# Performance work log

Measured on AMD Instinct MI355X. Metric: run time of the kernel, lower is better.

Reference implementation:

```python
import jax, jax.numpy as jnp
import numpy as np
import math

NUM_HEADS = 12
LN_EPS = 1e-5


def _band_mask(seq_len, level):
    # level 0 -> +/-2 window, level 1 -> +/-5 window, else full attention
    if level == 0:
        w = 2
    elif level == 1:
        w = 5
    else:
        return jnp.zeros((seq_len, seq_len), dtype=jnp.float32)
    i = jnp.arange(seq_len)
    inside = jnp.abs(i[:, None] - i[None, :]) <= w
    return jnp.where(inside, 0.0, -jnp.inf).astype(jnp.float32)


def setup_inputs() -> dict:
    key = jax.random.key(0)
    ks = jax.random.split(key, 8)
    B, S, H = 8, 1000, 768
    init = 0.02
    return {
        "features": jax.random.normal(ks[0], (B, S, H), jnp.float32),
        "pos_emb": jax.random.normal(ks[1], (1000, H), jnp.float32) * init,
        "Wq": jax.random.normal(ks[2], (H, H), jnp.float32) * init,
        "bq": jnp.zeros((H,), jnp.float32),
        "Wk": jax.random.normal(ks[3], (H, H), jnp.float32) * init,
        "bk": jnp.zeros((H,), jnp.float32),
        "Wv": jax.random.normal(ks[4], (H, H), jnp.float32) * init,
        "bv": jnp.zeros((H,), jnp.float32),
        "Wo": jax.random.normal(ks[5], (H, H), jnp.float32) * init,
        "bo": jnp.zeros((H,), jnp.float32),
        "ln_g": jnp.ones((H,), jnp.float32),
        "ln_b": jnp.zeros((H,), jnp.float32),
        "level": 0,
    }


def reference(features, pos_emb, Wq, bq, Wk, bk, Wv, bv, Wo, bo, ln_g, ln_b, level):
    B, S, H = features.shape
    nh = NUM_HEADS
    hd = H // nh
    # level-specific positional encoding (level_specific=True path)
    scale = 1.0 + 0.1 * level
    x = features + pos_emb[:S][None, :, :] * scale

    def proj(W, b):
        y = jnp.einsum('bsh,oh->bso', x, W) + b  # torch Linear: x @ W.T + b
        return y.reshape(B, S, nh, hd).transpose(0, 2, 1, 3)  # [B, nh, S, hd]

    Q = proj(Wq, bq)
    K = proj(Wk, bk)
    V = proj(Wv, bv)

    scores = jnp.einsum('bhqd,bhkd->bhqk', Q, K) / math.sqrt(hd)
    scores = scores + _band_mask(S, level)[None, None, :, :]
    attn = jax.nn.softmax(scores, axis=-1)  # dropout is identity (eval / p=0)
    ctx = jnp.einsum('bhqk,bhkd->bhqd', attn, V)
    ctx = ctx.transpose(0, 2, 1, 3).reshape(B, S, H)

    out = jnp.einsum('bsh,oh->bso', ctx, Wo) + bo
    y = out + features
    mu = jnp.mean(y, axis=-1, keepdims=True)
    var = jnp.var(y, axis=-1, keepdims=True)
    return (y - mu) / jnp.sqrt(var + LN_EPS) * ln_g + ln_b
```

## Files before the change

### kernel.cpp

```cpp
#include <hip/hip_runtime.h>
#include <hip/hip_bf16.h>
#include <cstddef>

typedef __attribute__((ext_vector_type(8))) short bf16x8;
typedef __attribute__((ext_vector_type(4))) float f32x4;

static __device__ __forceinline__ unsigned short f2bf(float f) {
    unsigned int u = __float_as_uint(f);
    u += 0x7fffu + ((u >> 16) & 1u);
    return (unsigned short)(u >> 16);
}
static __device__ __forceinline__ float bf2f(unsigned short h) {
    return __uint_as_float(((unsigned int)h) << 16);
}

#define B_ 8
#define S_ 1000
#define H_ 768
#define NH_ 12
#define HD_ 64
#define M_ 8000
#define HC_ 2304

__global__ __launch_bounds__(256)
void prep_all_kernel(const float* __restrict__ feat, const float* __restrict__ pos,
                     const int* __restrict__ level, unsigned short* __restrict__ xb,
                     const float* __restrict__ wq, const float* __restrict__ wk,
                     const float* __restrict__ wv, const float* __restrict__ wo,
                     unsigned short* __restrict__ wdst) {
    const size_t NX = (size_t)M_ * H_ / 4;
    const size_t WSZ = (size_t)H_ * H_;
    size_t gid = (size_t)blockIdx.x * blockDim.x + threadIdx.x;
    if (gid < NX) {
        size_t e = gid * 4;
        float sc = 1.0f + 0.1f * (float)level[0];
        const float4 f = *reinterpret_cast<const float4*>(&feat[e]);
        size_t pe = e % ((size_t)S_ * H_);
        const float4 p = *reinterpret_cast<const float4*>(&pos[pe]);
        ushort4 o;
        o.x = f2bf(f.x + sc * p.x);
        o.y = f2bf(f.y + sc * p.y);
        o.z = f2bf(f.z + sc * p.z);
        o.w = f2bf(f.w + sc * p.w);
        *reinterpret_cast<ushort4*>(&xb[e]) = o;
    } else {
        size_t e = (gid - NX) * 4;
        if (e >= 4 * WSZ) return;
        const float* src; size_t off;
        if (e < WSZ)          { src = wq; off = e; }
        else if (e < 2 * WSZ) { src = wk; off = e - WSZ; }
        else if (e < 3 * WSZ) { src = wv; off = e - 2 * WSZ; }
        else                  { src = wo; off = e - 3 * WSZ; }
        const float4 f = *reinterpret_cast<const float4*>(&src[off]);
        ushort4 o;
        o.x = f2bf(f.x); o.y = f2bf(f.y); o.z = f2bf(f.z); o.w = f2bf(f.w);
        *reinterpret_cast<ushort4*>(&wdst[e]) = o;
    }
}

__global__ __launch_bounds__(512, 4)
void gemm_qkv5(const unsigned short* __restrict__ A,
               const unsigned short* __restrict__ Bw,
               const float* __restrict__ b0, const float* __restrict__ b1,
               const float* __restrict__ b2,
               unsigned short* __restrict__ outB) {
    const int K = H_;
    __shared__ char lds[65536];
    const int tid = threadIdx.x, lane = tid & 63, wid = tid >> 6;
    const int wr = wid >> 2, wc = wid & 3;
    const int fr = lane & 15, fq = lane >> 4;

    const int nwg = gridDim.x;
    const int q = nwg >> 3, r = nwg & 7;
    const int xcd = blockIdx.x & 7, idx = blockIdx.x >> 3;
    const int swz = (xcd < r) ? (xcd * (q + 1) + idx) : (r * (q + 1) + (xcd - r) * q + idx);
    const int ntn = HC_ / 128;
    const int bm = (swz / ntn) * 128;
    const int bn = (swz % ntn) * 128;

    const int srow = lane >> 2;
    const int scol = ((lane & 3) ^ ((lane >> 3) & 3)) * 8;

    auto stage = [&](int buf, int k0) {
        char* base = lds + buf * 32768;
#pragma unroll
        for (int s = 0; s < 2; ++s) {
            char* half = base + s * 16384;
            const int kk = k0 + s * 32;
            int ar = bm + wid * 16 + srow;
            ar = ar < M_ ? ar : M_ - 1;
            __builtin_amdgcn_global_load_lds(
                (const __attribute__((address_space(1))) unsigned int*)(A + (size_t)ar * K + kk + scol),
                (__attribute__((address_space(3))) unsigned int*)(half + wid * 1024), 16, 0, 0);
            const int br = bn + wid * 16 + srow;
            __builtin_amdgcn_global_load_lds(
                (const __attribute__((address_space(1))) unsigned int*)(Bw + (size_t)br * K + kk + scol),
                (__attribute__((address_space(3))) unsigned int*)(half + 8192 + wid * 1024), 16, 0, 0);
        }
    };

    f32x4 acc[4][2] = {};
    const int rsl = fq ^ ((fr >> 1) & 3);
    const int NT = K / 64;

    stage(0, 0);
    for (int t = 0; t < NT; ++t) {
        const int cur = t & 1;
        if (t + 1 < NT) {
            stage(cur ^ 1, (t + 1) * 64);
            asm volatile("s_waitcnt vmcnt(4)" ::: "memory");
        } else {
            asm volatile("s_waitcnt vmcnt(0)" ::: "memory");
        }
        __builtin_amdgcn_s_barrier();

        char* base = lds + cur * 32768;
#pragma unroll
        for (int s = 0; s < 2; ++s) {
            char* half = base + s * 16384;
            bf16x8 af[4], bfv[2];
#pragma unroll
            for (int m = 0; m < 4; ++m) {
                const int row = wr * 64 + m * 16 + fr;
                af[m] = *reinterpret_cast<const bf16x8*>(half + row * 64 + rsl * 16);
            }
#pragma unroll
            for (int n = 0; n < 2; ++n) {
                const int row = wc * 32 + n * 16 + fr;
                bfv[n] = *reinterpret_cast<const bf16x8*>(half + 8192 + row * 64 + rsl * 16);
            }
            __builtin_amdgcn_s_setprio(1);
#pragma unroll
            for (int m = 0; m < 4; ++m)
#pragma unroll
                for (int n = 0; n < 2; ++n)
                    acc[m][n] = __builtin_amdgcn_mfma_f32_16x16x32_bf16(bfv[n], af[m], acc[m][n], 0, 0, 0);
            __builtin_amdgcn_s_setprio(0);
        }
        __builtin_amdgcn_s_barrier();
    }

    const int colg = (bn < 768) ? bn : (bn < 1536) ? bn - 768 : bn - 1536;
    const float* bsel = (bn < 768) ? b0 : (bn < 1536) ? b1 : b2;
#pragma unroll
    for (int m = 0; m < 4; ++m) {
        const int row = bm + wr * 64 + m * 16 + fr;
        if (row >= M_) continue;
#pragma unroll
        for (int n = 0; n < 2; ++n) {
            const int cb = wc * 32 + n * 16 + fq * 4;
            const float4 bv = *reinterpret_cast<const float4*>(&bsel[colg + cb]);
            ushort4 o;
            o.x = f2bf(acc[m][n][0] + bv.x);
            o.y = f2bf(acc[m][n][1] + bv.y);
            o.z = f2bf(acc[m][n][2] + bv.z);
            o.w = f2bf(acc[m][n][3] + bv.w);
            *reinterpret_cast<ushort4*>(&outB[(size_t)row * HC_ + bn + cb]) = o;
        }
    }
}

__global__ __launch_bounds__(256, 4)
void gemm_out4(const unsigned short* __restrict__ A,
               const unsigned short* __restrict__ Bw,
               const float* __restrict__ b0,
               const float* __restrict__ resid,
               float* __restrict__ outF) {
    const int K = H_;
    __shared__ char lds[49152];
    const int tid = threadIdx.x, lane = tid & 63, wid = tid >> 6;
    const int wr = wid >> 1, wc = wid & 1;
    const int fr = lane & 15, fq = lane >> 4;

    const int nwg = gridDim.x;
    const int q = nwg >> 3, r = nwg & 7;
    const int xcd = blockIdx.x & 7, idx = blockIdx.x >> 3;
    const int swz = (xcd < r) ? (xcd * (q + 1) + idx) : (r * (q + 1) + (xcd - r) * q + idx);
    const int ntn = H_ / 64;
    const int bm = (swz / ntn) * 128;
    const int bn = (swz % ntn) * 64;

    const int srow = lane >> 2;
    const int scol = ((lane & 3) ^ ((lane >> 3) & 3)) * 8;

    auto stage = [&](int buf, int k0) {
        char* base = lds + buf * 24576;
#pragma unroll
        for (int s = 0; s < 2; ++s) {
            char* half = base + s * 12288;
            const int kk = k0 + s * 32;
#pragma unroll
            for (int t = 0; t < 2; ++t) {
                const int c = wid * 2 + t;
                int ar = bm + c * 16 + srow;
                ar = ar < M_ ? ar : M_ - 1;
                __builtin_amdgcn_global_load_lds(
                    (const __attribute__((address_space(1))) unsigned int*)(A + (size_t)ar * K + kk + scol),
                    (__attribute__((address_space(3))) unsigned int*)(half + c * 1024), 16, 0, 0);
            }
            const int br = bn + wid * 16 + srow;
            __builtin_amdgcn_global_load_lds(
                (const __attribute__((address_space(1))) unsigned int*)(Bw + (size_t)br * K + kk + scol),
                (__attribute__((address_space(3))) unsigned int*)(half + 8192 + wid * 1024), 16, 0, 0);
        }
    };

    f32x4 acc[4][2] = {};
    const int rsl = fq ^ ((fr >> 1) & 3);
    const int NT = K / 64;

    stage(0, 0);
    for (int t = 0; t < NT; ++t) {
        const int cur = t & 1;
        if (t + 1 < NT) {
            stage(cur ^ 1, (t + 1) * 64);
            asm volatile("s_waitcnt vmcnt(6)" ::: "memory");
        } else {
            asm volatile("s_waitcnt vmcnt(0)" ::: "memory");
        }
        __builtin_amdgcn_s_barrier();

        char* base = lds + cur * 24576;
#pragma unroll
        for (int s = 0; s < 2; ++s) {
            char* half = base + s * 12288;
            bf16x8 af[4], bfv[2];
#pragma unroll
            for (int m = 0; m < 4; ++m) {
                const int row = wr * 64 + m * 16 + fr;
                af[m] = *reinterpret_cast<const bf16x8*>(half + row * 64 + rsl * 16);
            }
#pragma unroll
            for (int n = 0; n < 2; ++n) {
                const int row = wc * 32 + n * 16 + fr;
                bfv[n] = *reinterpret_cast<const bf16x8*>(half + 8192 + row * 64 + rsl * 16);
            }
            __builtin_amdgcn_s_setprio(1);
#pragma unroll
            for (int m = 0; m < 4; ++m)
#pragma unroll
                for (int n = 0; n < 2; ++n)
                    acc[m][n] = __builtin_amdgcn_mfma_f32_16x16x32_bf16(bfv[n], af[m], acc[m][n], 0, 0, 0);
            __builtin_amdgcn_s_setprio(0);
        }
        __builtin_amdgcn_s_barrier();
    }

#pragma unroll
    for (int m = 0; m < 4; ++m) {
        const int row = bm + wr * 64 + m * 16 + fr;
        if (row >= M_) continue;
#pragma unroll
        for (int n = 0; n < 2; ++n) {
            const int col = bn + wc * 32 + n * 16 + fq * 4;
            const float4 bv = *reinterpret_cast<const float4*>(&b0[col]);
            const float4 rv = *reinterpret_cast<const float4*>(&resid[(size_t)row * H_ + col]);
            float4 ov;
            ov.x = acc[m][n][0] + bv.x + rv.x;
            ov.y = acc[m][n][1] + bv.y + rv.y;
            ov.z = acc[m][n][2] + bv.z + rv.z;
            ov.w = acc[m][n][3] + bv.w + rv.w;
            *reinterpret_cast<float4*>(&outF[(size_t)row * H_ + col]) = ov;
        }
    }
}

__global__ __launch_bounds__(256)
void attn_kernel(const unsigned short* __restrict__ QKV,
                 unsigned short* __restrict__ ctx,
                 const int* __restrict__ level_p) {
    const int lane = threadIdx.x & 63;
    const int wv = threadIdx.x >> 6;
    const int qiw = lane >> 2;
    const int d0 = (lane & 3) * 16;

    const int qt = blockIdx.x & 15;
    const int h  = (blockIdx.x >> 4) % NH_;
    const int b  = blockIdx.x / (16 * NH_);
    const int i  = qt * 64 + wv * 16 + qiw;
    const bool valid = i < S_;
    const int iq = valid ? i : S_ - 1;

    const int lev = level_p[0];
    const int w = (lev == 0) ? 2 : (lev == 1) ? 5 : S_;

    const size_t qoff = (size_t)(b * S_ + iq) * HC_ + h * HD_ + d0;
    bf16x8 qa = *reinterpret_cast<const bf16x8*>(&QKV[qoff]);
    bf16x8 qb = *reinterpret_cast<const bf16x8*>(&QKV[qoff + 8]);
    float qf[16];
#pragma unroll
    for (int t = 0; t < 8; ++t) {
        qf[t]     = bf2f((unsigned short)qa[t]);
        qf[t + 8] = bf2f((unsigned short)qb[t]);
    }

    const int j0 = max(0, i - w), j1 = min(S_ - 1, i + w);
    float mx = -1e30f, l = 0.f;
    float acc[16];
#pragma unroll
    for (int t = 0; t < 16; ++t) acc[t] = 0.f;

    for (int jc = j0; jc <= j1; jc += 5) {
        float s[5];
        int jj[5];
#pragma unroll
        for (int t = 0; t < 5; ++t) {
            const int j = jc + t;
            jj[t] = j <= j1 ? j : j1;
            const size_t koff = (size_t)(b * S_ + jj[t]) * HC_ + 768 + h * HD_ + d0;
            bf16x8 ka = *reinterpret_cast<const bf16x8*>(&QKV[koff]);
            bf16x8 kb = *reinterpret_cast<const bf16x8*>(&QKV[koff + 8]);
            float p = 0.f;
#pragma unroll
            for (int d = 0; d < 8; ++d) {
                p = fmaf(qf[d], bf2f((unsigned short)ka[d]), p);
                p = fmaf(qf[d + 8], bf2f((unsigned short)kb[d]), p);
            }
            s[t] = p;
        }
#pragma unroll
        for (int t = 0; t < 5; ++t) s[t] += __shfl_xor(s[t], 1);
#pragma unroll
        for (int t = 0; t < 5; ++t) s[t] += __shfl_xor(s[t], 2);
#pragma unroll
        for (int t = 0; t < 5; ++t)
            s[t] = (jc + t <= j1) ? s[t] * 0.125f : -1e30f;

        float cm = fmaxf(fmaxf(fmaxf(s[0], s[1]), fmaxf(s[2], s[3])), s[4]);
        float nm = fmaxf(mx, cm);
        float corr = __expf(mx - nm);
        l *= corr;
#pragma unroll
        for (int t = 0; t < 16; ++t) acc[t] *= corr;
#pragma unroll
        for (int t = 0; t < 5; ++t) {
            const float e = __expf(s[t] - nm);
            l += e;
            const size_t voff = (size_t)(b * S_ + jj[t]) * HC_ + 1536 + h * HD_ + d0;
            bf16x8 va = *reinterpret_cast<const bf16x8*>(&QKV[voff]);
            bf16x8 vb = *reinterpret_cast<const bf16x8*>(&QKV[voff + 8]);
#pragma unroll
            for (int d = 0; d < 8; ++d) {
                acc[d]     = fmaf(e, bf2f((unsigned short)va[d]), acc[d]);
                acc[d + 8] = fmaf(e, bf2f((unsigned short)vb[d]), acc[d + 8]);
            }
        }
        mx = nm;
    }

    if (valid) {
        const float inv = 1.f / l;
        bf16x8 o0, o1;
#pragma unroll
        for (int t = 0; t < 8; ++t) {
            o0[t] = (short)f2bf(acc[t] * inv);
            o1[t] = (short)f2bf(acc[t + 8] * inv);
        }
        unsigned short* dst = &ctx[(size_t)(b * S_ + i) * H_ + h * HD_ + d0];
        *reinterpret_cast<bf16x8*>(dst) = o0;
        *reinterpret_cast<bf16x8*>(dst + 8) = o1;
    }
}

__global__ __launch_bounds__(256)
void ln_kernel(float* __restrict__ y, const float* __restrict__ g, const float* __restrict__ bta) {
    int row = blockIdx.x;
    int tid = threadIdx.x;
    float* p = y + (size_t)row * H_;
    float v[3];
    float s = 0.f, s2 = 0.f;
#pragma unroll
    for (int t = 0; t < 3; ++t) {
        v[t] = p[tid + t * 256];
        s += v[t];
        s2 += v[t] * v[t];
    }
#pragma unroll
    for (int o = 32; o; o >>= 1) {
        s  += __shfl_xor(s, o);
        s2 += __shfl_xor(s2, o);
    }
    __shared__ float ss[4], ss2[4];
    if ((tid & 63) == 0) { ss[tid >> 6] = s; ss2[tid >> 6] = s2; }
    __syncthreads();
    s  = ss[0] + ss[1] + ss[2] + ss[3];
    s2 = ss2[0] + ss2[1] + ss2[2] + ss2[3];
    float mu = s * (1.f / H_);
    float var = s2 * (1.f / H_) - mu * mu;
    float rs = rsqrtf(var + 1e-5f);
#pragma unroll
    for (int t = 0; t < 3; ++t) {
        int c = tid + t * 256;
        p[c] = (v[t] - mu) * rs * g[c] + bta[c];
    }
}

extern "C" void kernel_launch(void* const* d_in, const int* in_sizes, int n_in,
                              void* d_out, int out_size, void* d_ws, size_t ws_size,
                              hipStream_t stream) {
    const float* feat  = (const float*)d_in[0];
    const float* pos   = (const float*)d_in[1];
    const float* Wq    = (const float*)d_in[2];
    const float* bq    = (const float*)d_in[3];
    const float* Wk    = (const float*)d_in[4];
    const float* bk    = (const float*)d_in[5];
    const float* Wv    = (const float*)d_in[6];
    const float* bv    = (const float*)d_in[7];
    const float* Wo    = (const float*)d_in[8];
    const float* bo    = (const float*)d_in[9];
    const float* ln_g  = (const float*)d_in[10];
    const float* ln_b  = (const float*)d_in[11];
    const int*   level = (const int*)d_in[12];
    float* out = (float*)d_out;

    char* ws = (char*)d_ws;
    unsigned short* xb   = (unsigned short*)ws;
    unsigned short* Wcat = xb + (size_t)M_ * H_;
    unsigned short* QKVb = Wcat + (size_t)4 * H_ * H_;
    unsigned short* ctxb = QKVb + (size_t)M_ * HC_;

    const int nprep = (int)(((size_t)M_ * H_ / 4 + (size_t)4 * H_ * H_ / 4 + 255) / 256);
    prep_all_kernel<<<nprep, 256, 0, stream>>>(feat, pos, level, xb, Wq, Wk, Wv, Wo, Wcat);
    gemm_qkv5<<<63 * 18, 512, 0, stream>>>(xb, Wcat, bq, bk, bv, QKVb);
    attn_kernel<<<B_ * NH_ * 16, 256, 0, stream>>>(QKVb, ctxb, level);
    gemm_out4<<<63 * 12, 256, 0, stream>>>(ctxb, Wcat + (size_t)3 * H_ * H_, bo, feat, out);
    ln_kernel<<<M_, 256, 0, stream>>>(out, ln_g, ln_b);
}
```

Baseline: 106.8 us.

## Use a four-slot LDS ring with three-deep prefetch in QKV GEMM

Replaces the double-buffered 64-wide K loop in the QKV projection GEMM with a four-slot ring of 32-wide K stages. Loads for stage p+3 are issued right after the fragment reads for stage p. Each step then needs one barrier instead of two. The aim is to hide global-to-LDS latency behind more in-flight loads and to cut barrier stalls, at the cost of more loop iterations and finer-grained waitcnt bookkeeping.

New measurement: 108.4 us. No clear change (+1.5%).

```diff
diff --git a/kernel.cpp b/kernel.cpp
--- a/kernel.cpp
+++ b/kernel.cpp
@@ -59,7 +59,7 @@
 }
 
 __global__ __launch_bounds__(512, 4)
-void gemm_qkv5(const unsigned short* __restrict__ A,
+void gemm_qkv7(const unsigned short* __restrict__ A,
                const unsigned short* __restrict__ Bw,
                const float* __restrict__ b0, const float* __restrict__ b1,
                const float* __restrict__ b2,
@@ -81,63 +81,53 @@
     const int srow = lane >> 2;
     const int scol = ((lane & 3) ^ ((lane >> 3) & 3)) * 8;
 
-    auto stage = [&](int buf, int k0) {
-        char* base = lds + buf * 32768;
-#pragma unroll
-        for (int s = 0; s < 2; ++s) {
-            char* half = base + s * 16384;
-            const int kk = k0 + s * 32;
-            int ar = bm + wid * 16 + srow;
-            ar = ar < M_ ? ar : M_ - 1;
-            __builtin_amdgcn_global_load_lds(
-                (const __attribute__((address_space(1))) unsigned int*)(A + (size_t)ar * K + kk + scol),
-                (__attribute__((address_space(3))) unsigned int*)(half + wid * 1024), 16, 0, 0);
-            const int br = bn + wid * 16 + srow;
-            __builtin_amdgcn_global_load_lds(
-                (const __attribute__((address_space(1))) unsigned int*)(Bw + (size_t)br * K + kk + scol),
-                (__attribute__((address_space(3))) unsigned int*)(half + 8192 + wid * 1024), 16, 0, 0);
-        }
+    auto stage = [&](int p) {
+        char* base = lds + (p & 3) * 16384;
+        const int kk = p * 32;
+        int ar = bm + wid * 16 + srow;
+        ar = ar < M_ ? ar : M_ - 1;
+        __builtin_amdgcn_global_load_lds(
+            (const __attribute__((address_space(1))) unsigned int*)(A + (size_t)ar * K + kk + scol),
+            (__attribute__((address_space(3))) unsigned int*)(base + wid * 1024), 16, 0, 0);
+        const int br = bn + wid * 16 + srow;
+        __builtin_amdgcn_global_load_lds(
+            (const __attribute__((address_space(1))) unsigned int*)(Bw + (size_t)br * K + kk + scol),
+            (__attribute__((address_space(3))) unsigned int*)(base + 8192 + wid * 1024), 16, 0, 0);
     };
 
     f32x4 acc[4][2] = {};
     const int rsl = fq ^ ((fr >> 1) & 3);
-    const int NT = K / 64;
-
-    stage(0, 0);
-    for (int t = 0; t < NT; ++t) {
-        const int cur = t & 1;
-        if (t + 1 < NT) {
-            stage(cur ^ 1, (t + 1) * 64);
-            asm volatile("s_waitcnt vmcnt(4)" ::: "memory");
-        } else {
-            asm volatile("s_waitcnt vmcnt(0)" ::: "memory");
-        }
-        __builtin_amdgcn_s_barrier();
-
-        char* base = lds + cur * 32768;
-#pragma unroll
-        for (int s = 0; s < 2; ++s) {
-            char* half = base + s * 16384;
-            bf16x8 af[4], bfv[2];
-#pragma unroll
-            for (int m = 0; m < 4; ++m) {
-                const int row = wr * 64 + m * 16 + fr;
-                af[m] = *reinterpret_cast<const bf16x8*>(half + row * 64 + rsl * 16);
-            }
-#pragma unroll
-            for (int n = 0; n < 2; ++n) {
-                const int row = wc * 32 + n * 16 + fr;
-                bfv[n] = *reinterpret_cast<const bf16x8*>(half + 8192 + row * 64 + rsl * 16);
-            }
-            __builtin_amdgcn_s_setprio(1);
-#pragma unroll
-            for (int m = 0; m < 4; ++m)
-#pragma unroll
-                for (int n = 0; n < 2; ++n)
-                    acc[m][n] = __builtin_amdgcn_mfma_f32_16x16x32_bf16(bfv[n], af[m], acc[m][n], 0, 0, 0);
-            __builtin_amdgcn_s_setprio(0);
-        }
-        __builtin_amdgcn_s_barrier();
+    const int NP = K / 32;
+
+    stage(0); stage(1); stage(2);
+    asm volatile("s_waitcnt vmcnt(4)" ::: "memory");
+    __builtin_amdgcn_s_barrier();
+
+    for (int p = 0; p < NP; ++p) {
+        char* half = lds + (p & 3) * 16384;
+        bf16x8 af[4], bfv[2];
+#pragma unroll
+        for (int m = 0; m < 4; ++m) {
+            const int row = wr * 64 + m * 16 + fr;
+            af[m] = *reinterpret_cast<const bf16x8*>(half + row * 64 + rsl * 16);
+        }
+#pragma unroll
+        for (int n = 0; n < 2; ++n) {
+            const int row = wc * 32 + n * 16 + fr;
+            bfv[n] = *reinterpret_cast<const bf16x8*>(half + 8192 + row * 64 + rsl * 16);
+        }
+        if (p + 3 < NP) stage(p + 3);
+        __builtin_amdgcn_s_setprio(1);
+#pragma unroll
+        for (int m = 0; m < 4; ++m)
+#pragma unroll
+            for (int n = 0; n < 2; ++n)
+                acc[m][n] = __builtin_amdgcn_mfma_f32_16x16x32_bf16(bfv[n], af[m], acc[m][n], 0, 0, 0);
+        __builtin_amdgcn_s_setprio(0);
+        if (p + 3 < NP)       { asm volatile("s_waitcnt vmcnt(4)" ::: "memory"); }
+        else if (p == NP - 3) { asm volatile("s_waitcnt vmcnt(2)" ::: "memory"); }
+        else if (p == NP - 2) { asm volatile("s_waitcnt vmcnt(0)" ::: "memory"); }
+        if (p + 1 < NP) __builtin_amdgcn_s_barrier();
     }
 
     const int colg = (bn < 768) ? bn : (bn < 1536) ? bn - 768 : bn - 1536;
@@ -421,7 +411,7 @@
 
     const int nprep = (int)(((size_t)M_ * H_ / 4 + (size_t)4 * H_ * H_ / 4 + 255) / 256);
     prep_all_kernel<<<nprep, 256, 0, stream>>>(feat, pos, level, xb, Wq, Wk, Wv, Wo, Wcat);
-    gemm_qkv5<<<63 * 18, 512, 0, stream>>>(xb, Wcat, bq, bk, bv, QKVb);
+    gemm_qkv7<<<63 * 18, 512, 0, stream>>>(xb, Wcat, bq, bk, bv, QKVb);
     attn_kernel<<<B_ * NH_ * 16, 256, 0, stream>>>(QKVb, ctxb, level);
     gemm_out4<<<63 * 12, 256, 0, stream>>>(ctxb, Wcat + (size_t)3 * H_ * H_, bo, feat, out);
     ln_kernel<<<M_, 256, 0, stream>>>(out, ln_g, ln_b);
```
